# Optimization experiments

Hardware: AMD Instinct MI355X
Metric: run time of the kernel (lower is better)

## Reference

```python
import jax, jax.numpy as jnp
import numpy as np

B, ORDER, N, D, H = 16, 2, 512, 128, 8
DH = D // H
NEG_SLOPE = 0.2


def setup_inputs() -> dict:
    key = jax.random.key(0)
    ks = jax.random.split(key, 8)
    stdv = 1.0 / np.sqrt(DH)

    def u(k, shape):
        return jax.random.uniform(k, shape, jnp.float32, -stdv, stdv)

    x = jax.random.normal(ks[0], (B, ORDER, N, D), jnp.float32)
    A = jax.random.randint(ks[1], (B, ORDER, N, N), 0, 5, jnp.int32)
    # Stacked params for the 2*order GAT modules: axis0 = order, axis1 = (conv1, conv2)
    W = u(ks[2], (ORDER, 2, D, D))            # project.weight
    pb = jnp.zeros((ORDER, 2, D), jnp.float32)  # project.bias (init 0)
    att_src = u(ks[3], (ORDER, 2, H, DH))
    att_dst = u(ks[4], (ORDER, 2, H, DH))
    bias = jnp.zeros((ORDER, 2, D), jnp.float32)  # GAT output bias (init 0)
    return {"x": x, "A": A, "W": W, "pb": pb,
            "att_src": att_src, "att_dst": att_dst, "bias": bias}


def _gat(x, Af, W, pb, a_src, a_dst, b):
    # x: [B,N,D]; Af: [B,N,N] float in {0,1}
    xp = x @ W.T + pb                                  # project
    xh = xp.reshape(B, N, H, DH)                       # [B,N,H,DH]
    s_src = jnp.einsum('bnhd,hd->bnh', xh, a_src)      # [B,N,H]
    s_dst = jnp.einsum('bnhd,hd->bnh', xh, a_dst)
    alpha = s_src[:, :, None, :] + s_dst[:, None, :, :]  # [B,src,dst,H]
    alpha = jnp.where((Af != 1.0)[..., None], 0.0, alpha)
    alpha = jnp.where(alpha >= 0, alpha, NEG_SLOPE * alpha)  # leaky relu
    alpha = jax.nn.softmax(alpha, axis=1)              # softmax over src dim
    out = jnp.einsum('bsdh,bshf->bdhf', alpha, xh).reshape(B, N, D)
    out = out + xp                                     # add_self_loops
    return out + b


def reference(x, A, W, pb, att_src, att_dst, bias):
    A1 = ((A == 2) | (A == 4)).astype(x.dtype)  # [B,ORDER,N,N]
    A2 = ((A == 3) | (A == 4)).astype(x.dtype)
    hs = []
    for i in range(ORDER):
        h1 = _gat(x[:, i], A1[:, i], W[i, 0], pb[i, 0], att_src[i, 0], att_dst[i, 0], bias[i, 0])
        h2 = _gat(x[:, i], A2[:, i], W[i, 1], pb[i, 1], att_src[i, 1], att_dst[i, 1], bias[i, 1])
        hs.append(h1 + h2)
    h = jnp.stack(hs, axis=1)                          # [B,ORDER,N,D]
    out = h + h.mean(axis=1, keepdims=True)
    return out
```

## Files before the change

### kernel.cpp

```cpp
#include <hip/hip_runtime.h>

#define N_ 512
#define D_ 128
#define LOG2E 1.44269504088896f


typedef __attribute__((ext_vector_type(8))) short short8;
typedef __attribute__((ext_vector_type(4))) float floatx4;
typedef __attribute__((ext_vector_type(4))) unsigned int uintx4;
typedef __attribute__((ext_vector_type(2))) _Float16 half2v;
typedef __attribute__((ext_vector_type(8))) _Float16 half8;

#if defined(__has_builtin)
#if __has_builtin(__builtin_amdgcn_exp2f)
#define EXP2F(x) __builtin_amdgcn_exp2f(x)
#else
#define EXP2F(x) exp2f(x)
#endif
#else
#define EXP2F(x) exp2f(x)
#endif

__device__ __forceinline__ unsigned int pkh(float a, float b) {
    auto h = __builtin_amdgcn_cvt_pkrtz(a, b);
    return __builtin_bit_cast(unsigned int, h);
}

__global__ __launch_bounds__(256) void prep_kernel(
    const float* __restrict__ x, const float* __restrict__ W,
    const float* __restrict__ pb, const float* __restrict__ att_src,
    const float* __restrict__ att_dst, const int* __restrict__ A,
    unsigned short* __restrict__ xpt, unsigned int* __restrict__ sgEs,
    unsigned int* __restrict__ sgFs, float2* __restrict__ sgD,
    unsigned int* __restrict__ mgT)
{
    __shared__ _Float16 va_l[8][136];
    __shared__ float c0_l[8];

    const int bid0 = blockIdx.x;
    const int t = threadIdx.x;

    if (bid0 >= 1024) {
        const int bid = bid0 - 1024;
        const int bi = bid >> 4;
        const int rem = bid & 15;
        const int dg = rem >> 2;
        const int jw = rem & 3;
        const int dp = t & 63, q = t >> 6;
        const int dstb = dg * 128 + dp * 2;
        const int sbase = jw * 128 + q * 8;
        const int* Ab = A + (size_t)bi * N_ * N_ + dstb;
        unsigned int a00 = 0, a01 = 0, a10 = 0, a11 = 0;
#pragma unroll
        for (int cp = 0; cp < 4; ++cp) {
#pragma unroll
            for (int i = 0; i < 8; ++i) {
                const int s = sbase + cp * 32 + i;
                const int2 v = *(const int2*)(Ab + (size_t)s * N_);
                const int bitp = cp * 8 + i;
                a00 |= ((0x14u >> v.x) & 1u) << bitp;
                a10 |= ((0x18u >> v.x) & 1u) << bitp;
                a01 |= ((0x14u >> v.y) & 1u) << bitp;
                a11 |= ((0x18u >> v.y) & 1u) << bitp;
            }
        }
        const int i0 = bi * 2;
        mgT[(((size_t)i0 * 4 + q) * 512 + dstb + 0) * 4 + jw] = a00;
        mgT[(((size_t)i0 * 4 + q) * 512 + dstb + 1) * 4 + jw] = a01;
        mgT[(((size_t)(i0 + 1) * 4 + q) * 512 + dstb + 0) * 4 + jw] = a10;
        mgT[(((size_t)(i0 + 1) * 4 + q) * 512 + dstb + 1) * 4 + jw] = a11;
        return;
    }

    const int unit = bid0 >> 1;
    const int half = bid0 & 1;
    const int ntile = unit & 7;
    const int inst  = unit >> 3;
    const int j = inst & 1;
    const int bi = inst >> 1;
    const int ij = (bi & 1) * 2 + j;
    const int wave = t >> 6, L = t & 63, n = L & 15, q = L >> 4;
    const float* wb = W + (size_t)ij * D_ * D_;

    {
        const int c = t >> 5;
        const int k0 = (t & 31) * 4;
        const int hn = half * 4 + (c & 3);
        const float* av = ((c < 4) ? att_src : att_dst) + ij * D_ + hn * 16;
        const float* Wh = wb + (size_t)(hn * 16) * D_ + k0;
        float a0 = 0.f, a1 = 0.f, a2 = 0.f, a3 = 0.f;
#pragma unroll
        for (int dd = 0; dd < 16; ++dd) {
            const float a = av[dd];
            const float4 wv = *(const float4*)(Wh + (size_t)dd * D_);
            a0 += wv.x * a; a1 += wv.y * a; a2 += wv.z * a; a3 += wv.w * a;
        }
        va_l[c][k0 + 0] = (_Float16)(a0 * LOG2E);
        va_l[c][k0 + 1] = (_Float16)(a1 * LOG2E);
        va_l[c][k0 + 2] = (_Float16)(a2 * LOG2E);
        va_l[c][k0 + 3] = (_Float16)(a3 * LOG2E);
        if (t < 8) {
            const int hn2 = half * 4 + (t & 3);
            const float* av2 = ((t < 4) ? att_src : att_dst) + ij * D_ + hn2 * 16;
            const float* pbp = pb + ij * D_ + hn2 * 16;
            float s = 0.f;
#pragma unroll
            for (int dd = 0; dd < 16; ++dd) s += pbp[dd] * av2[dd];
            c0_l[t] = s * LOG2E;
        }
    }

    const int n0w = ntile * 64 + wave * 16;
    const float* xrow = x + ((size_t)bi * N_ + n0w + n) * D_ + q * 8;
    half8 Af[4];
#pragma unroll
    for (int kc = 0; kc < 4; ++kc) {
        const float4 a0 = *(const float4*)(xrow + kc * 32);
        const float4 a1 = *(const float4*)(xrow + kc * 32 + 4);
        uintx4 au;
        au.x = pkh(a0.x, a0.y);
        au.y = pkh(a0.z, a0.w);
        au.z = pkh(a1.x, a1.y);
        au.w = pkh(a1.z, a1.w);
        Af[kc] = __builtin_bit_cast(half8, au);
    }

    __syncthreads();

    floatx4 S = (floatx4){0.f, 0.f, 0.f, 0.f};
    {
        const _Float16* var = &va_l[n & 7][q * 8];
#pragma unroll
        for (int kc = 0; kc < 4; ++kc) {
            const half8 Bs = *(const half8*)(var + kc * 32);
            S = __builtin_amdgcn_mfma_f32_16x16x32_f16(Af[kc], Bs, S, 0, 0, 0);
        }
    }

#pragma unroll
    for (int ft = 0; ft < 4; ++ft) {
        const int head = half * 4 + ft;
        const int fg = head * 16 + n;
        const float* wrow = wb + (size_t)fg * D_ + q * 8;
        floatx4 C = (floatx4){0.f, 0.f, 0.f, 0.f};
#pragma unroll
        for (int kc = 0; kc < 4; ++kc) {
            const float4 b0 = *(const float4*)(wrow + kc * 32);
            const float4 b1 = *(const float4*)(wrow + kc * 32 + 4);
            uintx4 bu;
            bu.x = pkh(b0.x, b0.y);
            bu.y = pkh(b0.z, b0.w);
            bu.z = pkh(b1.x, b1.y);
            bu.w = pkh(b1.z, b1.w);
            C = __builtin_amdgcn_mfma_f32_16x16x32_f16(
                Af[kc], __builtin_bit_cast(half8, bu), C, 0, 0, 0);
        }
        const float pbv = pb[ij * D_ + fg];
        uint2 pk;
        pk.x = pkh(C[0] + pbv, C[1] + pbv);
        pk.y = pkh(C[2] + pbv, C[3] + pbv);
        *(uint2*)&xpt[((size_t)inst * D_ + fg) * N_ + n0w + q * 4] = pk;
    }

    if (n < 8) {
        const float cc = c0_l[n];
        const float v0 = S[0] + cc, v1 = S[1] + cc;
        const float v2 = S[2] + cc, v3 = S[3] + cc;
        if (n < 4) {
            const int head = half * 4 + n;
            const size_t base = ((size_t)inst * 8 + head) * 256 + (n0w >> 1) + q * 2;
            sgEs[base + 0] = pkh(EXP2F(v0), EXP2F(v1));
            sgEs[base + 1] = pkh(EXP2F(v2), EXP2F(v3));
            sgFs[base + 0] = pkh(EXP2F(0.2f * v0), EXP2F(0.2f * v1));
            sgFs[base + 1] = pkh(EXP2F(0.2f * v2), EXP2F(0.2f * v3));
        } else {
            const int head = half * 4 + (n - 4);
            const size_t base = ((size_t)inst * 8 + head) * N_ + n0w + q * 4;
            float2 e0; e0.x = EXP2F(v0); e0.y = EXP2F(0.2f * v0); sgD[base + 0] = e0;
            float2 e1; e1.x = EXP2F(v1); e1.y = EXP2F(0.2f * v1); sgD[base + 1] = e1;
            float2 e2; e2.x = EXP2F(v2); e2.y = EXP2F(0.2f * v2); sgD[base + 2] = e2;
            float2 e3; e3.x = EXP2F(v3); e3.y = EXP2F(0.2f * v3); sgD[base + 3] = e3;
        }
    }
}

__global__ __launch_bounds__(512, 8) void attn_kernel(
    const unsigned short* __restrict__ xpt,
    const unsigned int* __restrict__ sgEs,
    const unsigned int* __restrict__ sgFs,
    const float2* __restrict__ sgD,
    const unsigned int* __restrict__ mgT,
    const float* __restrict__ bias,
    float* __restrict__ hout)
{
    __shared__ unsigned int smem[8192];

    const int bid = blockIdx.x;
    const int xcd = bid & 7;
    const int idx = bid >> 3;
    const int bi  = xcd * 4 + (idx >> 5);
    const int tile = idx & 31;
    const int i0   = bi * 2;
    const int d0 = tile * 16;
    const int t = threadIdx.x;
    const int wave = t >> 6, L = t & 63, n = L & 15, q = L >> 4;
    const int cv = wave >> 2;
    const int h0 = (wave & 3) * 2;
    const int inst = i0 + cv;
    const int ij = (bi & 1) * 2 + cv;

    {
        const uint4* sE = (const uint4*)(sgEs + (size_t)i0 * 2048);
        const uint4* sF = (const uint4*)(sgFs + (size_t)i0 * 2048);
        uint4* dE = (uint4*)smem;
        uint4* dF = (uint4*)(smem + 4096);
        dE[t] = sE[t]; dE[512 + t] = sE[512 + t];
        dF[t] = sF[t]; dF[512 + t] = sF[512 + t];
    }

    const uint4 mreg = *(const uint4*)(mgT + (((size_t)inst * 4 + q) * 512 + d0 + n) * 4);
    const unsigned int mw_[4] = { mreg.x, mreg.y, mreg.z, mreg.w };

    unsigned int iEd2[2], rd2[2];
#pragma unroll
    for (int hh = 0; hh < 2; ++hh) {
        const float2 ed = sgD[((size_t)inst * 8 + h0 + hh) * N_ + d0 + n];
        const float iEd = 1.0f / ed.x;
        const float rdv = ed.y * iEd;
        iEd2[hh] = pkh(iEd, iEd);
        rd2[hh] = pkh(rdv, rdv);
    }

    __syncthreads();

    const unsigned short* xpi = xpt + (size_t)inst * D_ * N_;
    const unsigned short* bp0 = xpi + (size_t)(h0 * 16 + n) * N_;
    const unsigned short* bp1 = xpi + (size_t)((h0 + 1) * 16 + n) * N_;
    const unsigned int* esw = smem + cv * 2048;
    const unsigned int* fsw = smem + 4096 + cv * 2048;

    const uintx4 ou = { 0x3C003C00u, 0x3C003C00u, 0x3C003C00u, 0x3C003C00u };
    const half8 onesB = __builtin_bit_cast(half8, ou);

    floatx4 Cacc[2] = { (floatx4){0.f,0.f,0.f,0.f}, (floatx4){0.f,0.f,0.f,0.f} };
    floatx4 Cz[2]   = { (floatx4){0.f,0.f,0.f,0.f}, (floatx4){0.f,0.f,0.f,0.f} };

    uintx4 A0 = *(const uintx4*)(bp0 + q * 8);
    uintx4 A1 = *(const uintx4*)(bp1 + q * 8);
    uintx4 P0 = *(const uintx4*)(bp0 + 32 + q * 8);
    uintx4 P1 = *(const uintx4*)(bp1 + 32 + q * 8);
#pragma unroll
    for (int c = 0; c < 16; ++c) {
        uintx4 F0, F1;
        if (c < 14) {
            F0 = *(const uintx4*)(bp0 + (c + 2) * 32 + q * 8);
            F1 = *(const uintx4*)(bp1 + (c + 2) * 32 + q * 8);
        }
        const unsigned int word = mw_[c >> 2];
        unsigned int sel[4];
#pragma unroll
        for (int p = 0; p < 4; ++p) {
            const int sh = (c & 3) * 8 + 2 * p;
            const unsigned int wb2 = word >> sh;
            sel[p] = ((wb2 & 1u) ? 0x0000FFFFu : 0u) |
                     ((wb2 & 2u) ? 0xFFFF0000u : 0u);
        }
        const int spb = c * 16 + q * 4;
#pragma unroll
        for (int hh = 0; hh < 2; ++hh) {
            const uint4 Ep = *(const uint4*)&esw[(h0 + hh) * 256 + spb];
            const uint4 Fp = *(const uint4*)&fsw[(h0 + hh) * 256 + spb];
            const unsigned int eu[4] = { Ep.x, Ep.y, Ep.z, Ep.w };
            const unsigned int fu[4] = { Fp.x, Fp.y, Fp.z, Fp.w };
            const half2v rdh = __builtin_bit_cast(half2v, rd2[hh]);
            uintx4 au;
            unsigned int wts[4];
#pragma unroll
            for (int p = 0; p < 4; ++p) {
                const half2v e = __builtin_bit_cast(half2v, eu[p]);
                const half2v f = __builtin_bit_cast(half2v, fu[p]);
                const half2v pr = f * rdh;
                const half2v wv = __builtin_elementwise_max(pr, e);
                const unsigned int wvu = __builtin_bit_cast(unsigned int, wv);
                wts[p] = (sel[p] & wvu) | (~sel[p] & iEd2[hh]);
            }
            au.x = wts[0]; au.y = wts[1]; au.z = wts[2]; au.w = wts[3];
            const half8 As = __builtin_bit_cast(half8, au);
            Cacc[hh] = __builtin_amdgcn_mfma_f32_16x16x32_f16(
                As, __builtin_bit_cast(half8, hh ? A1 : A0), Cacc[hh], 0, 0, 0);
            Cz[hh] = __builtin_amdgcn_mfma_f32_16x16x32_f16(
                As, onesB, Cz[hh], 0, 0, 0);
        }
        A0 = P0; A1 = P1;
        P0 = F0; P1 = F1;
    }

    float vals[2][4];
#pragma unroll
    for (int hh = 0; hh < 2; ++hh) {
        const int h = h0 + hh;
        const float bv = bias[ij * D_ + h * 16 + n];
        const uint2 sv = *(const uint2*)(xpi + (size_t)(h * 16 + n) * N_ + d0 + q * 4);
        const half2v s0 = __builtin_bit_cast(half2v, sv.x);
        const half2v s1 = __builtin_bit_cast(half2v, sv.y);
        const float selfv[4] = { (float)s0[0], (float)s0[1],
                                 (float)s1[0], (float)s1[1] };
#pragma unroll
        for (int reg = 0; reg < 4; ++reg) {
            const float Zi = 1.0f / Cz[hh][reg];
            vals[hh][reg] = Cacc[hh][reg] * Zi + selfv[reg] + bv;
        }
    }

    __syncthreads();
    float* out_l = (float*)smem;
    if (cv == 1) {
#pragma unroll
        for (int hh = 0; hh < 2; ++hh)
#pragma unroll
            for (int reg = 0; reg < 4; ++reg)
                out_l[(q * 4 + reg) * 132 + (h0 + hh) * 16 + n] = vals[hh][reg];
    }
    __syncthreads();
    if (cv == 0) {
#pragma unroll
        for (int hh = 0; hh < 2; ++hh)
#pragma unroll
            for (int reg = 0; reg < 4; ++reg)
                hout[((size_t)bi * N_ + d0 + q * 4 + reg) * D_ + (h0 + hh) * 16 + n] =
                    vals[hh][reg] + out_l[(q * 4 + reg) * 132 + (h0 + hh) * 16 + n];
    }
}

__global__ __launch_bounds__(256) void combine_kernel(float* __restrict__ h)
{
    const int idx = blockIdx.x * 256 + threadIdx.x;
    const int b = idx >> 14;
    const int r = idx & 16383;
    float4* p0 = (float4*)h + (size_t)b * 32768 + r;
    float4* p1 = p0 + 16384;
    const float4 a = *p0;
    const float4 o = *p1;
    float4 r0, r1;
    r0.x = 1.5f * a.x + 0.5f * o.x;  r1.x = 1.5f * o.x + 0.5f * a.x;
    r0.y = 1.5f * a.y + 0.5f * o.y;  r1.y = 1.5f * o.y + 0.5f * a.y;
    r0.z = 1.5f * a.z + 0.5f * o.z;  r1.z = 1.5f * o.z + 0.5f * a.z;
    r0.w = 1.5f * a.w + 0.5f * o.w;  r1.w = 1.5f * o.w + 0.5f * a.w;
    *p0 = r0;
    *p1 = r1;
}

extern "C" void kernel_launch(void* const* d_in, const int* in_sizes, int n_in,
                              void* d_out, int out_size, void* d_ws, size_t ws_size,
                              hipStream_t stream)
{
    const float* x   = (const float*)d_in[0];
    const int*   A   = (const int*)d_in[1];
    const float* W   = (const float*)d_in[2];
    const float* pb  = (const float*)d_in[3];
    const float* as_ = (const float*)d_in[4];
    const float* ad_ = (const float*)d_in[5];
    const float* bs  = (const float*)d_in[6];

    unsigned short* xpt = (unsigned short*)d_ws;
    unsigned int* sgEs = (unsigned int*)((char*)d_ws + (8u << 20));
    unsigned int* sgFs = (unsigned int*)((char*)d_ws + (8u << 20) + (512u << 10));
    float2* sgD = (float2*)((char*)d_ws + (9u << 20));
    unsigned int* mgT = (unsigned int*)((char*)d_ws + (11u << 20));
    float* h = (float*)d_out;

    prep_kernel<<<1536, 256, 0, stream>>>(x, W, pb, as_, ad_, A, xpt, sgEs, sgFs, sgD, mgT);
    attn_kernel<<<1024, 512, 0, stream>>>(xpt, sgEs, sgFs, sgD, mgT, bs, h);
    combine_kernel<<<1024, 256, 0, stream>>>(h);
}
```

Baseline: 150.6 us.

## Fuse order-mean combine into attention kernel using 1024-thread blocks

The attention kernel now processes both orders (four GAT instances) of a batch element in one 1024-thread block. The cross-order mean is computed through shared memory before the final store, so the separate combine kernel and its read-modify-write pass over the output are gone. In exchange the grid halves to 512 blocks with doubled shared memory per block, which may reduce occupancy and latency hiding.

```diff
diff --git a/kernel.cpp b/kernel.cpp
--- a/kernel.cpp
+++ b/kernel.cpp
@@ -184,7 +184,7 @@
     }
 }
 
-__global__ __launch_bounds__(512, 8) void attn_kernel(
+__global__ __launch_bounds__(1024, 8) void attn_kernel(
     const unsigned short* __restrict__ xpt,
     const unsigned int* __restrict__ sgEs,
     const unsigned int* __restrict__ sgFs,
@@ -193,29 +193,31 @@
     const float* __restrict__ bias,
     float* __restrict__ hout)
 {
-    __shared__ unsigned int smem[8192];
+    __shared__ unsigned int smem[16384];
 
     const int bid = blockIdx.x;
     const int xcd = bid & 7;
     const int idx = bid >> 3;
-    const int bi  = xcd * 4 + (idx >> 5);
+    const int b   = xcd * 2 + (idx >> 5);
     const int tile = idx & 31;
-    const int i0   = bi * 2;
+    const int b4  = b * 4;
     const int d0 = tile * 16;
     const int t = threadIdx.x;
     const int wave = t >> 6, L = t & 63, n = L & 15, q = L >> 4;
-    const int cv = wave >> 2;
+    const int io = wave >> 3;
+    const int cv = (wave >> 2) & 1;
     const int h0 = (wave & 3) * 2;
-    const int inst = i0 + cv;
-    const int ij = (bi & 1) * 2 + cv;
+    const int il = io * 2 + cv;
+    const int inst = b4 + il;
+    const int ij = il;
 
     {
-        const uint4* sE = (const uint4*)(sgEs + (size_t)i0 * 2048);
-        const uint4* sF = (const uint4*)(sgFs + (size_t)i0 * 2048);
+        const uint4* sE = (const uint4*)(sgEs + (size_t)b4 * 2048);
+        const uint4* sF = (const uint4*)(sgFs + (size_t)b4 * 2048);
         uint4* dE = (uint4*)smem;
-        uint4* dF = (uint4*)(smem + 4096);
-        dE[t] = sE[t]; dE[512 + t] = sE[512 + t];
-        dF[t] = sF[t]; dF[512 + t] = sF[512 + t];
+        uint4* dF = (uint4*)(smem + 8192);
+        dE[t] = sE[t]; dE[1024 + t] = sE[1024 + t];
+        dF[t] = sF[t]; dF[1024 + t] = sF[1024 + t];
     }
 
     const uint4 mreg = *(const uint4*)(mgT + (((size_t)inst * 4 + q) * 512 + d0 + n) * 4);
@@ -236,8 +238,8 @@
     const unsigned short* xpi = xpt + (size_t)inst * D_ * N_;
     const unsigned short* bp0 = xpi + (size_t)(h0 * 16 + n) * N_;
     const unsigned short* bp1 = xpi + (size_t)((h0 + 1) * 16 + n) * N_;
-    const unsigned int* esw = smem + cv * 2048;
-    const unsigned int* fsw = smem + 4096 + cv * 2048;
+    const unsigned int* esw = smem + il * 2048;
+    const unsigned int* fsw = smem + 8192 + il * 2048;
 
     const uintx4 ou = { 0x3C003C00u, 0x3C003C00u, 0x3C003C00u, 0x3C003C00u };
     const half8 onesB = __builtin_bit_cast(half8, ou);
@@ -313,7 +315,7 @@
     }
 
     __syncthreads();
-    float* out_l = (float*)smem;
+    float* out_l = (float*)smem + io * 2112;
     if (cv == 1) {
 #pragma unroll
         for (int hh = 0; hh < 2; ++hh)
@@ -326,28 +328,23 @@
 #pragma unroll
         for (int hh = 0; hh < 2; ++hh)
 #pragma unroll
-            for (int reg = 0; reg < 4; ++reg)
-                hout[((size_t)bi * N_ + d0 + q * 4 + reg) * D_ + (h0 + hh) * 16 + n] =
-                    vals[hh][reg] + out_l[(q * 4 + reg) * 132 + (h0 + hh) * 16 + n];
-    }
-}
-
-__global__ __launch_bounds__(256) void combine_kernel(float* __restrict__ h)
-{
-    const int idx = blockIdx.x * 256 + threadIdx.x;
-    const int b = idx >> 14;
-    const int r = idx & 16383;
-    float4* p0 = (float4*)h + (size_t)b * 32768 + r;
-    float4* p1 = p0 + 16384;
-    const float4 a = *p0;
-    const float4 o = *p1;
-    float4 r0, r1;
-    r0.x = 1.5f * a.x + 0.5f * o.x;  r1.x = 1.5f * o.x + 0.5f * a.x;
-    r0.y = 1.5f * a.y + 0.5f * o.y;  r1.y = 1.5f * o.y + 0.5f * a.y;
-    r0.z = 1.5f * a.z + 0.5f * o.z;  r1.z = 1.5f * o.z + 0.5f * a.z;
-    r0.w = 1.5f * a.w + 0.5f * o.w;  r1.w = 1.5f * o.w + 0.5f * a.w;
-    *p0 = r0;
-    *p1 = r1;
+            for (int reg = 0; reg < 4; ++reg) {
+                vals[hh][reg] += out_l[(q * 4 + reg) * 132 + (h0 + hh) * 16 + n];
+                out_l[(q * 4 + reg) * 132 + (h0 + hh) * 16 + n] = vals[hh][reg];
+            }
+    }
+    __syncthreads();
+    if (cv == 0) {
+        const float* oth = (const float*)smem + (1 - io) * 2112;
+#pragma unroll
+        for (int hh = 0; hh < 2; ++hh)
+#pragma unroll
+            for (int reg = 0; reg < 4; ++reg) {
+                const float other = oth[(q * 4 + reg) * 132 + (h0 + hh) * 16 + n];
+                hout[((size_t)(b * 2 + io) * N_ + d0 + q * 4 + reg) * D_ +
+                     (h0 + hh) * 16 + n] = 1.5f * vals[hh][reg] + 0.5f * other;
+            }
+    }
 }
 
 extern "C" void kernel_launch(void* const* d_in, const int* in_sizes, int n_in,
@@ -370,6 +367,5 @@
     float* h = (float*)d_out;
 
     prep_kernel<<<1536, 256, 0, stream>>>(x, W, pb, as_, ad_, A, xpt, sgEs, sgFs, sgD, mgT);
-    attn_kernel<<<1024, 512, 0, stream>>>(xpt, sgEs, sgFs, sgD, mgT, bs, h);
-    combine_kernel<<<1024, 256, 0, stream>>>(h);
+    attn_kernel<<<512, 1024, 0, stream>>>(xpt, sgEs, sgFs, sgD, mgT, bs, h);
 }
```

After: 146.3 us. 2.8% less time.
